# Optimization experiments

Measured on AMD Instinct MI355X. Metric: run time of the kernel, lower is better.

## Reference

```python
import jax, jax.numpy as jnp
import numpy as np

BATCH, NODES, CH_IN, CH_OUT, N_EXPERTS = 8, 8192, 128, 128, 64

def setup_inputs() -> dict:
    key = jax.random.key(0)
    kx, kw, ks = jax.random.split(key, 3)
    x = jax.random.normal(kx, (BATCH, NODES, CH_IN), dtype=jnp.float32)
    # std = fan_in**-0.5 per self_init
    W = jax.random.normal(kw, (N_EXPERTS, CH_OUT, CH_IN), dtype=jnp.float32) * (CH_IN ** -0.5)
    sel = jax.random.randint(ks, (NODES,), 0, N_EXPERTS, dtype=jnp.int64)
    return {"x": x, "sel": sel, "W": W}

def reference(x, sel, W):
    # x: (b, n, j), W[sel]: (n, i, j) -> out: (b, n, i)
    Wsel = W[sel]  # gather a (ch_out, ch_in) matrix per node
    return jnp.einsum('bnj,nij->bni', x, Wsel)
```

## Files before the change

### kernel.cpp

```cpp
#include <hip/hip_runtime.h>

#define BATCH   8
#define NODES   8192
#define CH      128
#define NEXP    64
#define TN      16
#define MAXP    (NODES + NEXP * TN)
#define NTILES  (MAXP / TN)

typedef __attribute__((ext_vector_type(8))) short bf16x8;
typedef __attribute__((ext_vector_type(4))) float f32x4;

__device__ __forceinline__ bf16x8 cvt8(f32x4 lo, f32x4 hi) {
    bf16x8 r;
    #pragma unroll
    for (int i = 0; i < 4; ++i) {
        r[i]     = (short)__builtin_bit_cast(unsigned short, static_cast<__bf16>(lo[i]));
        r[i + 4] = (short)__builtin_bit_cast(unsigned short, static_cast<__bf16>(hi[i]));
    }
    return r;
}

__global__ __launch_bounds__(256)
void prep_kernel(const int* __restrict__ sel, const float* __restrict__ W,
                 short* __restrict__ Wbf, int* __restrict__ sorted)
{
    const int t = threadIdx.x;

    {
        const size_t base = (size_t)blockIdx.x * (CH * CH / 4);
        const float* ws = W   + base;
        short*       wd = Wbf + base;
        #pragma unroll
        for (int i = 0; i < 2; ++i) {
            int idx = (i * 256 + t) * 8;
            f32x4 lo = *reinterpret_cast<const f32x4*>(ws + idx);
            f32x4 hi = *reinterpret_cast<const f32x4*>(ws + idx + 4);
            *reinterpret_cast<bf16x8*>(wd + idx) = cvt8(lo, hi);
        }
    }

    const int e = blockIdx.x;
    if (e >= NEXP) return;

    const int wv = t >> 6;
    __shared__ int wcnt[4][NEXP];
    __shared__ int s_off, s_cnt, s_total, cursor;
    if (t < NEXP) { wcnt[0][t] = 0; wcnt[1][t] = 0; wcnt[2][t] = 0; wcnt[3][t] = 0; }
    if (t == 0) cursor = 0;
    __syncthreads();

    int myv[NODES / 256];
    #pragma unroll
    for (int i = 0; i < NODES / 256; ++i) {
        myv[i] = sel[i * 256 + t];
        atomicAdd(&wcnt[wv][myv[i]], 1);
    }
    __syncthreads();

    if (t < NEXP) {
        int c = wcnt[0][t] + wcnt[1][t] + wcnt[2][t] + wcnt[3][t];
        int p = (c + TN - 1) & ~(TN - 1);
        int scan = p;
        #pragma unroll
        for (int d = 1; d < NEXP; d <<= 1) {
            int v = __shfl_up(scan, d);
            if (t >= d) scan += v;
        }
        if (t == e)        { s_off = scan - p; s_cnt = c; }
        if (t == NEXP - 1) s_total = scan;
    }
    __syncthreads();

    const int off = s_off, myc = s_cnt;
    const int pad = (myc + TN - 1) & ~(TN - 1);

    for (int i = myc + t; i < pad; i += 256) sorted[off + i] = -1;

    if (e == NEXP - 1) {
        for (int i = s_total + t; i < MAXP; i += 256) sorted[i] = -1;
    }

    #pragma unroll
    for (int i = 0; i < NODES / 256; ++i) {
        if (myv[i] == e) {
            int pos = atomicAdd(&cursor, 1);
            sorted[off + pos] = i * 256 + t;
        }
    }
}

__global__ __launch_bounds__(256)
void gemm_kernel(const float* __restrict__ x, const int* __restrict__ sel,
                 const short* __restrict__ Wbf, float* __restrict__ out,
                 const int* __restrict__ sorted)
{
    __shared__ int s_nodes[TN];
    __shared__ int s_expert;

    const int tid  = threadIdx.x;
    const int tile = blockIdx.x;

    if (tid < TN) s_nodes[tid] = sorted[tile * TN + tid];
    if (tid == 0) {
        int n0 = sorted[tile * TN];
        s_expert = (n0 >= 0) ? sel[n0] : -1;
    }
    __syncthreads();

    const int e = s_expert;
    if (e < 0) return;

    const int wave = tid >> 6;
    const int lane = tid & 63;
    const int m16  = lane & 15;
    const int quad = lane >> 4;

    int          nodej[2];
    const float* xrow[2];
    #pragma unroll
    for (int jt = 0; jt < 2; ++jt) {
        int j    = wave * 32 + jt * 16 + m16;
        int node = s_nodes[j >> 3];
        int b    = j & 7;
        nodej[jt] = node;
        int nd   = (node >= 0) ? node : 0;
        xrow[jt] = x + ((size_t)(b * NODES + nd)) * CH;
    }
    const short* wbase = Wbf + (size_t)e * CH * CH;

    f32x4 acc[2][8];
    #pragma unroll
    for (int jt = 0; jt < 2; ++jt)
        #pragma unroll
        for (int ct = 0; ct < 8; ++ct)
            acc[jt][ct] = (f32x4){0.f, 0.f, 0.f, 0.f};

    #pragma unroll
    for (int kk = 0; kk < 4; ++kk) {
        const int k0 = kk * 32 + quad * 8;

        bf16x8 xfrag[2];
        #pragma unroll
        for (int jt = 0; jt < 2; ++jt) {
            const float* p = xrow[jt] + k0;
            f32x4 lo = *reinterpret_cast<const f32x4*>(p);
            f32x4 hi = *reinterpret_cast<const f32x4*>(p + 4);
            xfrag[jt] = cvt8(lo, hi);
        }

        #pragma unroll
        for (int ct = 0; ct < 8; ++ct) {
            bf16x8 wfrag = *reinterpret_cast<const bf16x8*>(
                wbase + (size_t)(ct * 16 + m16) * CH + k0);
            acc[0][ct] = __builtin_amdgcn_mfma_f32_16x16x32_bf16(
                             wfrag, xfrag[0], acc[0][ct], 0, 0, 0);
            acc[1][ct] = __builtin_amdgcn_mfma_f32_16x16x32_bf16(
                             wfrag, xfrag[1], acc[1][ct], 0, 0, 0);
        }
    }

    #pragma unroll
    for (int jt = 0; jt < 2; ++jt) {
        int node = nodej[jt];
        if (node < 0) continue;
        int j = wave * 32 + jt * 16 + m16;
        int b = j & 7;
        float* orow = out + ((size_t)(b * NODES + node)) * CH;
        #pragma unroll
        for (int ct = 0; ct < 8; ++ct)
            *reinterpret_cast<f32x4*>(orow + ct * 16 + quad * 4) = acc[jt][ct];
    }
}

extern "C" void kernel_launch(void* const* d_in, const int* in_sizes, int n_in,
                              void* d_out, int out_size, void* d_ws, size_t ws_size,
                              hipStream_t stream)
{
    const float* x   = (const float*)d_in[0];
    const int*   sel = (const int*)  d_in[1];
    const float* W   = (const float*)d_in[2];
    float*       out = (float*)d_out;

    short* Wbf    = (short*)d_ws;
    int*   sorted = (int*)((char*)d_ws + (size_t)NEXP * CH * CH * sizeof(short));

    prep_kernel<<<256, 256, 0, stream>>>(sel, W, Wbf, sorted);
    gemm_kernel<<<NTILES, 256, 0, stream>>>(x, sel, Wbf, out, sorted);
}
```

Baseline: 116.8 us.

## Split expert bucketing into per-slice histogram and scatter kernels

Replaces the per-expert sort, in which each of 64 blocks scanned all 8192 selectors, with a two-pass counting sort. The first kernel converts W to bf16, fills the sorted buffer with -1, and builds per-slice expert histograms. A second kernel computes padded expert offsets plus per-slice prefixes and scatters node indices through shared-memory atomics. This removes redundant full scans of sel, at the cost of an extra kernel launch and a global histogram round trip.

Measured after the change: 110.4 us. 5.4% less time.

```diff
diff --git a/kernel.cpp b/kernel.cpp
--- a/kernel.cpp
+++ b/kernel.cpp
@@ -7,6 +7,8 @@
 #define TN      16
 #define MAXP    (NODES + NEXP * TN)
 #define NTILES  (MAXP / TN)
+#define NSORT   64
+#define SLICE   (NODES / NSORT)
 
 typedef __attribute__((ext_vector_type(8))) short bf16x8;
 typedef __attribute__((ext_vector_type(4))) float f32x4;
@@ -22,13 +24,15 @@
 }
 
 __global__ __launch_bounds__(256)
-void prep_kernel(const int* __restrict__ sel, const float* __restrict__ W,
-                 short* __restrict__ Wbf, int* __restrict__ sorted)
+void prep1_kernel(const int* __restrict__ sel, const float* __restrict__ W,
+                  short* __restrict__ Wbf, int* __restrict__ sorted,
+                  int* __restrict__ gcnt)
 {
-    const int t = threadIdx.x;
+    const int t   = threadIdx.x;
+    const int blk = blockIdx.x;
 
     {
-        const size_t base = (size_t)blockIdx.x * (CH * CH / 4);
+        const size_t base = (size_t)blk * (CH * CH / 4);
         const float* ws = W   + base;
         short*       wd = Wbf + base;
         #pragma unroll
@@ -40,53 +44,53 @@
         }
     }
 
-    const int e = blockIdx.x;
-    if (e >= NEXP) return;
+    {
+        const int si = blk * 256 + t;
+        if (si < MAXP) sorted[si] = -1;
+    }
 
-    const int wv = t >> 6;
-    __shared__ int wcnt[4][NEXP];
-    __shared__ int s_off, s_cnt, s_total, cursor;
-    if (t < NEXP) { wcnt[0][t] = 0; wcnt[1][t] = 0; wcnt[2][t] = 0; wcnt[3][t] = 0; }
-    if (t == 0) cursor = 0;
-    __syncthreads();
+    if (blk < NSORT) {
+        __shared__ int hist[NEXP];
+        if (t < NEXP) hist[t] = 0;
+        __syncthreads();
+        if (t < SLICE) atomicAdd(&hist[sel[blk * SLICE + t]], 1);
+        __syncthreads();
+        if (t < NEXP) gcnt[blk * NEXP + t] = hist[t];
+    }
+}
 
-    int myv[NODES / 256];
-    #pragma unroll
-    for (int i = 0; i < NODES / 256; ++i) {
-        myv[i] = sel[i * 256 + t];
-        atomicAdd(&wcnt[wv][myv[i]], 1);
-    }
-    __syncthreads();
+__global__ __launch_bounds__(256)
+void prep2_kernel(const int* __restrict__ sel, const int* __restrict__ gcnt,
+                  int* __restrict__ sorted)
+{
+    const int t   = threadIdx.x;
+    const int blk = blockIdx.x;
+
+    __shared__ int cursor[NEXP];
 
     if (t < NEXP) {
-        int c = wcnt[0][t] + wcnt[1][t] + wcnt[2][t] + wcnt[3][t];
-        int p = (c + TN - 1) & ~(TN - 1);
+        int cnt = 0, own = 0;
+        for (int s = 0; s < NSORT; ++s) {
+            int g = gcnt[s * NEXP + t];
+            own += (s < blk) ? g : 0;
+            cnt += g;
+        }
+        int p = (cnt + TN - 1) & ~(TN - 1);
         int scan = p;
         #pragma unroll
         for (int d = 1; d < NEXP; d <<= 1) {
             int v = __shfl_up(scan, d);
             if (t >= d) scan += v;
         }
-        if (t == e)        { s_off = scan - p; s_cnt = c; }
-        if (t == NEXP - 1) s_total = scan;
+        cursor[t] = (scan - p) + own;
     }
     __syncthreads();
 
-    const int off = s_off, myc = s_cnt;
-    const int pad = (myc + TN - 1) & ~(TN - 1);
-
-    for (int i = myc + t; i < pad; i += 256) sorted[off + i] = -1;
-
-    if (e == NEXP - 1) {
-        for (int i = s_total + t; i < MAXP; i += 256) sorted[i] = -1;
-    }
-
-    #pragma unroll
-    for (int i = 0; i < NODES / 256; ++i) {
-        if (myv[i] == e) {
-            int pos = atomicAdd(&cursor, 1);
-            sorted[off + pos] = i * 256 + t;
-        }
+    if (t < SLICE) {
+        int n = blk * SLICE + t;
+        int e = sel[n];
+        int pos = atomicAdd(&cursor[e], 1);
+        sorted[pos] = n;
     }
 }
 
@@ -184,7 +188,9 @@
 
     short* Wbf    = (short*)d_ws;
     int*   sorted = (int*)((char*)d_ws + (size_t)NEXP * CH * CH * sizeof(short));
+    int*   gcnt   = sorted + MAXP;
 
-    prep_kernel<<<256, 256, 0, stream>>>(sel, W, Wbf, sorted);
+    prep1_kernel<<<256, 256, 0, stream>>>(sel, W, Wbf, sorted, gcnt);
+    prep2_kernel<<<NSORT, 256, 0, stream>>>(sel, gcnt, sorted);
     gemm_kernel<<<NTILES, 256, 0, stream>>>(x, sel, Wbf, out, sorted);
 }
```
